# Kernel tuning notes

Hardware: AMD Instinct MI355X
Metric: run time of the kernel (lower is better)

The kernel has to match this reference:

```python
import jax, jax.numpy as jnp
import numpy as np

BLOCK_SIZE = 64
HIDDEN = 1024
INTERMEDIATE = 4096
NUM_BLOCK = HIDDEN // BLOCK_SIZE              # 16
INT_BLOCK = (INTERMEDIATE // HIDDEN) * BLOCK_SIZE  # 256


def setup_inputs() -> dict:
    key = jax.random.key(0)
    k_x, k_w1, k_b1, k_w2, k_b2 = jax.random.split(key, 5)
    hidden_states = jax.random.normal(k_x, (4, 2048, HIDDEN), dtype=jnp.float32)
    w1 = 0.02 * jax.random.normal(k_w1, (NUM_BLOCK, INT_BLOCK, BLOCK_SIZE), dtype=jnp.float32)
    b1 = 0.001 * jax.random.normal(k_b1, (INTERMEDIATE,), dtype=jnp.float32)
    w2 = 0.02 * jax.random.normal(k_w2, (NUM_BLOCK, BLOCK_SIZE, INT_BLOCK), dtype=jnp.float32)
    b2 = 0.001 * jax.random.normal(k_b2, (HIDDEN,), dtype=jnp.float32)
    return {"hidden_states": hidden_states, "w1": w1, "b1": b1, "w2": w2, "b2": b2}


def reference(hidden_states, w1, b1, w2, b2):
    lead = hidden_states.shape[:-1]
    dim = hidden_states.shape[-1]
    nb, ibs, bs = w1.shape  # num_block, intermediate_block_size, block_size
    x = hidden_states.reshape(-1, nb, bs)                 # [B, n, i]
    h = jnp.einsum('bni,noi->bno', x, w1)                 # [B, n, o]
    # channel shuffle: transpose block and feature axes before flattening
    h = jnp.swapaxes(h, -1, -2).reshape(-1, nb * ibs)     # [B, o*n order]
    h = jax.nn.gelu(h + b1, approximate=False)
    h = h.reshape(-1, nb, ibs)                            # regroup after shuffle
    y = jnp.einsum('bni,noi->bno', h, w2).reshape(-1, nb * bs) + b2
    return y.reshape(*lead, dim)
```

## Files before the change

### kernel.cpp

```cpp
#include <hip/hip_runtime.h>
#include <hip/hip_bf16.h>


#define LDSK 256
#define CHUNK (16 * LDSK)

typedef __attribute__((ext_vector_type(8))) short  short8;
typedef __attribute__((ext_vector_type(4))) short  short4v;
typedef __attribute__((ext_vector_type(4))) float  floatx4;

__device__ __forceinline__ short f2bf(float f) {
  union { __hip_bfloat16 h; short s; } u;
  u.h = __float2bfloat16(f);
  return u.s;
}

__device__ __forceinline__ float gelu_f(float v) {
  float v2 = v * v;
  float p  = fmaf(0.044715f, v2, 1.0f);
  float t  = v * p;
  float e  = __expf(-1.5957691f * t);
  return v * __builtin_amdgcn_rcpf(1.0f + e);
}

__global__ void pack_w1_k(const float* __restrict__ w1, short* __restrict__ w1p) {
  const int t = blockIdx.x * blockDim.x + threadIdx.x;
  const int lane = t & 63, ks = (t >> 6) & 1, np = (t >> 7) & 15, n = (t >> 11) & 15;
  const int o  = np * 16 + (lane & 15);
  const int kb = ks * 32 + (lane >> 4) * 8;
  const float* src = w1 + ((size_t)(n * 256 + o) * 64 + kb);
  short8 f;
#pragma unroll
  for (int e = 0; e < 8; ++e) f[e] = f2bf(src[e]);
  *(short8*)(w1p + (size_t)t * 8) = f;
}

__global__ void pack_w2_k(const float* __restrict__ w2, short* __restrict__ w2p) {
  const int t = blockIdx.x * blockDim.x + threadIdx.x;
  const int lane = t & 63, ot = (t >> 6) & 3, ks = (t >> 8) & 7, np = (t >> 11) & 15;
  const int op = ot * 16 + (lane & 15);
  short8 f;
#pragma unroll
  for (int e = 0; e < 8; ++e) {
    const int k = ks * 32 + (lane >> 4) * 8 + e;
    const int n = k >> 4, ohi = k & 15;
    f[e] = f2bf(w2[(size_t)(np * 64 + op) * 256 + ohi * 16 + n]);
  }
  *(short8*)(w2p + (size_t)t * 8) = f;
}

__global__ __launch_bounds__(256, 4) void fused_k(
    const float* __restrict__ x, const float* __restrict__ b1,
    const float* __restrict__ b2, const short* __restrict__ w1p,
    const short* __restrict__ w2p, float* __restrict__ y) {
  __shared__ __align__(16) short hlds[2 * CHUNK];

  const int tid  = threadIdx.x;
  const int wv   = tid >> 6;
  const int lane = tid & 63;
  const int l15  = lane & 15;
  const int lhi  = lane >> 4;
  const int q    = blockIdx.x & 1;
  const int row0 = (blockIdx.x >> 1) * 16;
  const int np0  = q * 8;
  const int sw   = (l15 & 3) << 4;

  short8 xf[4][2];
#pragma unroll
  for (int bi = 0; bi < 4; ++bi) {
    const int n = 4 * wv + bi;
#pragma unroll
    for (int ks = 0; ks < 2; ++ks) {
      const float* px = x + (size_t)(row0 + l15) * 1024 + n * 64 + ks * 32 + lhi * 8;
      floatx4 a = *(const floatx4*)px;
      floatx4 b = *(const floatx4*)(px + 4);
      short8 f;
#pragma unroll
      for (int e = 0; e < 4; ++e) { f[e] = f2bf(a[e]); f[e + 4] = f2bf(b[e]); }
      xf[bi][ks] = f;
    }
  }

#pragma unroll
  for (int it = 0; it < 8; ++it) {
    const int np = np0 + it;
    short* buf = hlds + (it & 1) * CHUNK;

    short8 bf[8];
#pragma unroll
    for (int ks = 0; ks < 8; ++ks)
      bf[ks] = *(const short8*)(w2p + (size_t)(((np * 8 + ks) * 4 + wv) * 64 + lane) * 8);

#pragma unroll
    for (int bi = 0; bi < 4; ++bi) {
      const int n = 4 * wv + bi;
      short8 wf0 = *(const short8*)(w1p + (size_t)(((n * 16 + np) * 2 + 0) * 64 + lane) * 8);
      short8 wf1 = *(const short8*)(w1p + (size_t)(((n * 16 + np) * 2 + 1) * 64 + lane) * 8);
      float bias[4];
#pragma unroll
      for (int r = 0; r < 4; ++r)
        bias[r] = b1[np * 256 + (lhi * 4 + r) * 16 + n];
      floatx4 acc = {0.f, 0.f, 0.f, 0.f};
      acc = __builtin_amdgcn_mfma_f32_16x16x32_bf16(wf0, xf[bi][0], acc, 0, 0, 0);
      acc = __builtin_amdgcn_mfma_f32_16x16x32_bf16(wf1, xf[bi][1], acc, 0, 0, 0);
      short4v hv;
#pragma unroll
      for (int r = 0; r < 4; ++r)
        hv[r] = f2bf(gelu_f(acc[r] + bias[r]));
      *(short4v*)(&buf[l15 * LDSK + ((n * 16 + lhi * 4) ^ sw)]) = hv;
    }
    __syncthreads();

    floatx4 a0 = {0.f, 0.f, 0.f, 0.f}, a1 = {0.f, 0.f, 0.f, 0.f};
    const short* arow = &buf[l15 * LDSK];
#pragma unroll
    for (int ks = 0; ks < 8; ks += 2) {
      short8 f0 = *(const short8*)(arow + (((ks + 0) * 32 + lhi * 8) ^ sw));
      short8 f1 = *(const short8*)(arow + (((ks + 1) * 32 + lhi * 8) ^ sw));
      a0 = __builtin_amdgcn_mfma_f32_16x16x32_bf16(f0, bf[ks], a0, 0, 0, 0);
      a1 = __builtin_amdgcn_mfma_f32_16x16x32_bf16(f1, bf[ks + 1], a1, 0, 0, 0);
    }
    const int col = np * 64 + wv * 16 + l15;
    const float bb = b2[col];
    float* py = y + (size_t)(row0 + lhi * 4) * 1024 + col;
#pragma unroll
    for (int r = 0; r < 4; ++r)
      py[(size_t)r * 1024] = a0[r] + a1[r] + bb;
  }
}

extern "C" void kernel_launch(void* const* d_in, const int* in_sizes, int n_in,
                              void* d_out, int out_size, void* d_ws, size_t ws_size,
                              hipStream_t stream) {
  const float* x  = (const float*)d_in[0];
  const float* w1 = (const float*)d_in[1];
  const float* b1 = (const float*)d_in[2];
  const float* w2 = (const float*)d_in[3];
  const float* b2 = (const float*)d_in[4];
  float* y = (float*)d_out;

  short* w1p = (short*)d_ws;
  short* w2p = w1p + 16 * 256 * 64;

  pack_w1_k<<<64, 512, 0, stream>>>(w1, w1p);
  pack_w2_k<<<64, 512, 0, stream>>>(w2, w2p);
  fused_k<<<1024, 256, 0, stream>>>(x, b1, b2, w1p, w2p, y);
}
```

Before: 50.26 us.

## Split fused MLP into two GEMM kernels via global bf16 intermediate buffer

Replaces the single fused kernel, which staged the shuffled GELU activations in LDS with barriers, with two kernels. The first computes the block GEMM1 plus GELU and writes bf16 activations to a global workspace in the shuffled layout. The second reads them back for GEMM2. It also merges the weight packing kernels into one and pre-packs b1 into a vector-friendly layout. This removes the LDS traffic and __syncthreads, at the cost of a 64MB bf16 round trip through global memory/cache plus an extra launch.

```diff
diff --git a/kernel.cpp b/kernel.cpp
--- a/kernel.cpp
+++ b/kernel.cpp
@@ -1,9 +1,6 @@
 #include <hip/hip_runtime.h>
 #include <hip/hip_bf16.h>
 
-
-#define LDSK 256
-#define CHUNK (16 * LDSK)
 
 typedef __attribute__((ext_vector_type(8))) short  short8;
 typedef __attribute__((ext_vector_type(4))) short  short4v;
@@ -23,106 +20,106 @@
   return v * __builtin_amdgcn_rcpf(1.0f + e);
 }
 
-__global__ void pack_w1_k(const float* __restrict__ w1, short* __restrict__ w1p) {
+__global__ void pack_k(const float* __restrict__ w1, const float* __restrict__ w2,
+                       const float* __restrict__ b1, short* __restrict__ w1p,
+                       short* __restrict__ w2p, float* __restrict__ b1p) {
   const int t = blockIdx.x * blockDim.x + threadIdx.x;
-  const int lane = t & 63, ks = (t >> 6) & 1, np = (t >> 7) & 15, n = (t >> 11) & 15;
-  const int o  = np * 16 + (lane & 15);
-  const int kb = ks * 32 + (lane >> 4) * 8;
-  const float* src = w1 + ((size_t)(n * 256 + o) * 64 + kb);
-  short8 f;
+  const int lane = t & 63;
+  const int lhi = lane >> 4;
+  if (t < 32768) {
+    const int ks = (t >> 6) & 1, np = (t >> 7) & 15, n = (t >> 11) & 15;
+    const float* src = w1 + ((size_t)(n * 256 + np * 16 + (lane & 15)) * 64 + ks * 32 + lhi * 8);
+    short8 f;
 #pragma unroll
-  for (int e = 0; e < 8; ++e) f[e] = f2bf(src[e]);
-  *(short8*)(w1p + (size_t)t * 8) = f;
+    for (int e = 0; e < 8; ++e) f[e] = f2bf(src[e]);
+    *(short8*)(w1p + (size_t)t * 8) = f;
+  } else if (t < 65536) {
+    const int t2 = t - 32768;
+    const int ot = (t2 >> 6) & 3, ks = (t2 >> 8) & 7, np = (t2 >> 11) & 15;
+    const int op = ot * 16 + (lane & 15);
+    short8 f;
+#pragma unroll
+    for (int e = 0; e < 8; ++e) {
+      const int k = ks * 32 + lhi * 8 + e;
+      f[e] = f2bf(w2[(size_t)(np * 64 + op) * 256 + (k & 15) * 16 + (k >> 4)]);
+    }
+    *(short8*)(w2p + (size_t)t2 * 8) = f;
+  } else {
+    const int t3 = t - 65536;
+    const int np = (t3 >> 6) & 15, n = (t3 >> 10) & 15;
+    floatx4 b;
+#pragma unroll
+    for (int r = 0; r < 4; ++r) b[r] = b1[(np * 16 + lhi * 4 + r) * 16 + n];
+    *(floatx4*)(b1p + (size_t)((n * 16 + np) * 64 + lane) * 4) = b;
+  }
 }
 
-__global__ void pack_w2_k(const float* __restrict__ w2, short* __restrict__ w2p) {
-  const int t = blockIdx.x * blockDim.x + threadIdx.x;
-  const int lane = t & 63, ot = (t >> 6) & 3, ks = (t >> 8) & 7, np = (t >> 11) & 15;
-  const int op = ot * 16 + (lane & 15);
-  short8 f;
+__global__ __launch_bounds__(256, 4) void k1_gemm1(
+    const float* __restrict__ x, const short* __restrict__ w1p,
+    const float* __restrict__ b1p, short* __restrict__ G) {
+  const int tid = threadIdx.x;
+  const int wv = tid >> 6, lane = tid & 63;
+  const int l15 = lane & 15, lhi = lane >> 4;
+  const int rt = blockIdx.x >> 2;
+  const int n  = (blockIdx.x & 3) * 4 + wv;
+
+  short8 xf[2];
 #pragma unroll
-  for (int e = 0; e < 8; ++e) {
-    const int k = ks * 32 + (lane >> 4) * 8 + e;
-    const int n = k >> 4, ohi = k & 15;
-    f[e] = f2bf(w2[(size_t)(np * 64 + op) * 256 + ohi * 16 + n]);
+  for (int ks = 0; ks < 2; ++ks) {
+    const float* px = x + (size_t)(rt * 16 + l15) * 1024 + n * 64 + ks * 32 + lhi * 8;
+    floatx4 a = *(const floatx4*)px;
+    floatx4 b = *(const floatx4*)(px + 4);
+    short8 f;
+#pragma unroll
+    for (int e = 0; e < 4; ++e) { f[e] = f2bf(a[e]); f[e + 4] = f2bf(b[e]); }
+    xf[ks] = f;
   }
-  *(short8*)(w2p + (size_t)t * 8) = f;
+
+  short* gbase = G + (size_t)rt * 65536 + n * 256 + l15 * 16 + lhi * 4;
+#pragma unroll
+  for (int np = 0; np < 16; ++np) {
+    short8 wf0 = *(const short8*)(w1p + (size_t)(((n * 16 + np) * 2 + 0) * 64 + lane) * 8);
+    short8 wf1 = *(const short8*)(w1p + (size_t)(((n * 16 + np) * 2 + 1) * 64 + lane) * 8);
+    floatx4 bias = *(const floatx4*)(b1p + (size_t)((n * 16 + np) * 64 + lane) * 4);
+    floatx4 acc = {0.f, 0.f, 0.f, 0.f};
+    acc = __builtin_amdgcn_mfma_f32_16x16x32_bf16(wf0, xf[0], acc, 0, 0, 0);
+    acc = __builtin_amdgcn_mfma_f32_16x16x32_bf16(wf1, xf[1], acc, 0, 0, 0);
+    short4v hv;
+#pragma unroll
+    for (int r = 0; r < 4; ++r)
+      hv[r] = f2bf(gelu_f(acc[r] + bias[r]));
+    *(short4v*)(gbase + (size_t)np * 4096) = hv;
+  }
 }
 
-__global__ __launch_bounds__(256, 4) void fused_k(
-    const float* __restrict__ x, const float* __restrict__ b1,
-    const float* __restrict__ b2, const short* __restrict__ w1p,
-    const short* __restrict__ w2p, float* __restrict__ y) {
-  __shared__ __align__(16) short hlds[2 * CHUNK];
+__global__ __launch_bounds__(256, 4) void k2_gemm2(
+    const short* __restrict__ G, const short* __restrict__ w2p,
+    const float* __restrict__ b2, float* __restrict__ y) {
+  const int tid = threadIdx.x;
+  const int wv = tid >> 6, lane = tid & 63;
+  const int l15 = lane & 15, lhi = lane >> 4;
+  const int rt = blockIdx.x >> 2;
+  const int np = (blockIdx.x & 3) * 4 + wv;
 
-  const int tid  = threadIdx.x;
-  const int wv   = tid >> 6;
-  const int lane = tid & 63;
-  const int l15  = lane & 15;
-  const int lhi  = lane >> 4;
-  const int q    = blockIdx.x & 1;
-  const int row0 = (blockIdx.x >> 1) * 16;
-  const int np0  = q * 8;
-  const int sw   = (l15 & 3) << 4;
-
-  short8 xf[4][2];
+  const short* ab = G + (size_t)(rt * 16 + np) * 4096 + (lhi >> 1) * 256 + l15 * 16 + (lhi & 1) * 8;
+  short8 af[8];
 #pragma unroll
-  for (int bi = 0; bi < 4; ++bi) {
-    const int n = 4 * wv + bi;
-#pragma unroll
-    for (int ks = 0; ks < 2; ++ks) {
-      const float* px = x + (size_t)(row0 + l15) * 1024 + n * 64 + ks * 32 + lhi * 8;
-      floatx4 a = *(const floatx4*)px;
-      floatx4 b = *(const floatx4*)(px + 4);
-      short8 f;
-#pragma unroll
-      for (int e = 0; e < 4; ++e) { f[e] = f2bf(a[e]); f[e + 4] = f2bf(b[e]); }
-      xf[bi][ks] = f;
-    }
-  }
+  for (int ks = 0; ks < 8; ++ks)
+    af[ks] = *(const short8*)(ab + ks * 512);
 
 #pragma unroll
-  for (int it = 0; it < 8; ++it) {
-    const int np = np0 + it;
-    short* buf = hlds + (it & 1) * CHUNK;
-
-    short8 bf[8];
-#pragma unroll
-    for (int ks = 0; ks < 8; ++ks)
-      bf[ks] = *(const short8*)(w2p + (size_t)(((np * 8 + ks) * 4 + wv) * 64 + lane) * 8);
-
-#pragma unroll
-    for (int bi = 0; bi < 4; ++bi) {
-      const int n = 4 * wv + bi;
-      short8 wf0 = *(const short8*)(w1p + (size_t)(((n * 16 + np) * 2 + 0) * 64 + lane) * 8);
-      short8 wf1 = *(const short8*)(w1p + (size_t)(((n * 16 + np) * 2 + 1) * 64 + lane) * 8);
-      float bias[4];
-#pragma unroll
-      for (int r = 0; r < 4; ++r)
-        bias[r] = b1[np * 256 + (lhi * 4 + r) * 16 + n];
-      floatx4 acc = {0.f, 0.f, 0.f, 0.f};
-      acc = __builtin_amdgcn_mfma_f32_16x16x32_bf16(wf0, xf[bi][0], acc, 0, 0, 0);
-      acc = __builtin_amdgcn_mfma_f32_16x16x32_bf16(wf1, xf[bi][1], acc, 0, 0, 0);
-      short4v hv;
-#pragma unroll
-      for (int r = 0; r < 4; ++r)
-        hv[r] = f2bf(gelu_f(acc[r] + bias[r]));
-      *(short4v*)(&buf[l15 * LDSK + ((n * 16 + lhi * 4) ^ sw)]) = hv;
-    }
-    __syncthreads();
-
+  for (int ot = 0; ot < 4; ++ot) {
     floatx4 a0 = {0.f, 0.f, 0.f, 0.f}, a1 = {0.f, 0.f, 0.f, 0.f};
-    const short* arow = &buf[l15 * LDSK];
 #pragma unroll
     for (int ks = 0; ks < 8; ks += 2) {
-      short8 f0 = *(const short8*)(arow + (((ks + 0) * 32 + lhi * 8) ^ sw));
-      short8 f1 = *(const short8*)(arow + (((ks + 1) * 32 + lhi * 8) ^ sw));
-      a0 = __builtin_amdgcn_mfma_f32_16x16x32_bf16(f0, bf[ks], a0, 0, 0, 0);
-      a1 = __builtin_amdgcn_mfma_f32_16x16x32_bf16(f1, bf[ks + 1], a1, 0, 0, 0);
+      short8 b0 = *(const short8*)(w2p + (size_t)(((np * 8 + ks) * 4 + ot) * 64 + lane) * 8);
+      short8 b1f = *(const short8*)(w2p + (size_t)(((np * 8 + ks + 1) * 4 + ot) * 64 + lane) * 8);
+      a0 = __builtin_amdgcn_mfma_f32_16x16x32_bf16(af[ks], b0, a0, 0, 0, 0);
+      a1 = __builtin_amdgcn_mfma_f32_16x16x32_bf16(af[ks + 1], b1f, a1, 0, 0, 0);
     }
-    const int col = np * 64 + wv * 16 + l15;
+    const int col = np * 64 + ot * 16 + l15;
     const float bb = b2[col];
-    float* py = y + (size_t)(row0 + lhi * 4) * 1024 + col;
+    float* py = y + (size_t)(rt * 16 + lhi * 4) * 1024 + col;
 #pragma unroll
     for (int r = 0; r < 4; ++r)
       py[(size_t)r * 1024] = a0[r] + a1[r] + bb;
@@ -141,8 +138,10 @@
 
   short* w1p = (short*)d_ws;
   short* w2p = w1p + 16 * 256 * 64;
+  float* b1p = (float*)(w2p + 16 * 256 * 64);
+  short* G   = (short*)(b1p + 16 * 16 * 64 * 4);
 
-  pack_w1_k<<<64, 512, 0, stream>>>(w1, w1p);
-  pack_w2_k<<<64, 512, 0, stream>>>(w2, w2p);
-  fused_k<<<1024, 256, 0, stream>>>(x, b1, b2, w1p, w2p, y);
+  pack_k<<<160, 512, 0, stream>>>(w1, w2, b1, w1p, w2p, b1p);
+  k1_gemm1<<<2048, 256, 0, stream>>>(x, w1p, b1p, G);
+  k2_gemm2<<<2048, 256, 0, stream>>>(G, w2p, b2, y);
 }
```

New measurement: 53.58 us. +6.6%, slower.
